# Performance work log

Measured on AMD Instinct MI355X. Metric: run time of the kernel, lower is better.

The kernel has to match this reference:

```python
import jax, jax.numpy as jnp
import numpy as np

B, N, C = 128, 36, 1024
K_NB = 16            # neighbors per node (top-k, includes loop)
KERNEL = 8           # number of Gaussian kernels
OUT = 1024           # out_dim; per-kernel out = OUT // KERNEL
PI = np.float32(np.pi)


def setup_inputs() -> dict:
    key = jax.random.key(0)
    ks = jax.random.split(key, 9)
    node_feats = jax.random.normal(ks[0], (B, N, C), dtype=jnp.float32)
    node_centre = jax.random.uniform(ks[1], (B, N, 2), dtype=jnp.float32)
    neighbor_idx = jax.random.randint(ks[2], (B * N, K_NB), 0, B * N, dtype=jnp.int32)
    graph_weights = jax.random.uniform(ks[3], (B * N * K_NB, 1), dtype=jnp.float32)
    # Gaussian kernel params (per reset_parameters)
    mean_rho = jax.random.uniform(ks[4], (1, KERNEL), dtype=jnp.float32)
    mean_theta = jax.random.uniform(ks[5], (1, KERNEL), minval=-PI, maxval=PI, dtype=jnp.float32)
    precision_rho = jax.random.uniform(ks[6], (1, KERNEL), minval=0.5, maxval=1.0, dtype=jnp.float32)
    precision_theta = jax.random.uniform(ks[7], (1, KERNEL), minval=0.5, maxval=1.0, dtype=jnp.float32)
    # per-kernel Linear(node_dim, out_dim//kernel, bias=False), stacked: [K, d_out_k, C]
    conv_w = jax.random.normal(ks[8], (KERNEL, OUT // KERNEL, C), dtype=jnp.float32) * (1.0 / np.sqrt(C))
    return {
        "node_feats": node_feats,
        "node_centre": node_centre,
        "neighbor_idx": neighbor_idx,
        "graph_weights": graph_weights,
        "mean_rho": mean_rho,
        "mean_theta": mean_theta,
        "precision_rho": precision_rho,
        "precision_theta": precision_theta,
        "conv_w": conv_w,
    }


def _forward(node_feats, node_centre, graph_weights,
             mean_rho, mean_theta, precision_rho, precision_theta,
             conv_w, neighbor_idx):
    b, n, c = node_feats.shape
    bn = b * n
    # pseudo polar coordinates per edge: centre_i - centre_j
    centre = node_centre.reshape(bn, 2)                       # [BN, 2]
    diff = centre[:, None, :] - centre[neighbor_idx]          # [BN, K_nb, 2]
    coord_x = diff[..., 0].reshape(-1)                        # [E]
    coord_y = diff[..., 1].reshape(-1)
    rho = jnp.sqrt(coord_x ** 2 + coord_y ** 2)
    theta = jnp.arctan2(coord_x, coord_y)
    # Gaussian mixture membership weights over KERNEL kernels
    w_rho = jnp.exp(-0.5 * (rho[:, None] - mean_rho) ** 2 / (1e-14 + precision_rho ** 2))
    first_angle = jnp.abs(theta[:, None] - mean_theta)
    second_angle = jnp.abs(2.0 * PI - first_angle)
    w_theta = jnp.exp(-0.5 * jnp.minimum(first_angle, second_angle) ** 2 / (1e-14 + precision_theta ** 2))
    weights = w_rho * w_theta                                  # [E, KERNEL]
    weights = jnp.where(jnp.isnan(weights), 0.0, weights)
    weights = weights / jnp.sum(weights, axis=1, keepdims=True)
    # combine with graph edge weights
    edge_w = graph_weights * weights                           # [E, KERNEL]
    edge_w = edge_w.reshape(bn, K_NB, KERNEL).transpose(0, 2, 1)  # [BN, K, K_nb]
    # gather neighbor features and weighted aggregate (bmm)
    nbr = node_feats.reshape(bn, c)[neighbor_idx]              # [BN, K_nb, C]
    agg = jnp.einsum('ekn,enc->ekc', edge_w, nbr)              # [BN, KERNEL, C]
    agg = agg.reshape(b, n, KERNEL, c)
    # per-kernel linear then concat over kernel dim
    out = jnp.einsum('bnkc,kdc->bnkd', agg, conv_w)            # [B, N, KERNEL, OUT//KERNEL]
    out = out.reshape(b, n, -1)                                # [B, N, OUT]
    return jax.nn.relu(out)


def reference(node_feats, node_centre, neighbor_idx, graph_weights,
              mean_rho, mean_theta, precision_rho, precision_theta, conv_w):
    return _forward(node_feats, node_centre, graph_weights,
                    mean_rho, mean_theta, precision_rho, precision_theta,
                    conv_w, neighbor_idx)
```

## Files before the change

kernel.cpp:

```cpp
#include <hip/hip_runtime.h>
#include <hip/hip_bf16.h>
#include <stdint.h>

#define B_DIM   128
#define N_DIM   36
#define C_DIM   1024
#define KNB     16
#define NKER    8
#define OUTD    1024
#define BN_NODES (B_DIM * N_DIM)
#define E_EDGES  (BN_NODES * KNB)
#define PI_F 3.14159265358979323846f

typedef __attribute__((ext_vector_type(8))) short bf16x8;
typedef __attribute__((ext_vector_type(4))) float floatx4;

struct alignas(8) U16x4 { unsigned short x, y, z, w; };

__device__ __forceinline__ unsigned short f2bf(float f) {
  union { float f; uint32_t u; } v; v.f = f;
  uint32_t u = v.u;
  return (unsigned short)((u + 0x7fffu + ((u >> 16) & 1u)) >> 16);
}
__device__ __forceinline__ float bf2f(unsigned short h) {
  union { uint32_t u; float f; } v; v.u = ((uint32_t)h) << 16;
  return v.f;
}

__device__ __forceinline__ void gload16(const void* g, void* l) {
  __builtin_amdgcn_global_load_lds((__attribute__((address_space(1))) void*)(g),
                                   (__attribute__((address_space(3))) void*)(l),
                                   16, 0, 0);
}

#define VMCNT(n) asm volatile("s_waitcnt vmcnt(" #n ")" ::: "memory")
#define LGKM0()  asm volatile("s_waitcnt lgkmcnt(0)" ::: "memory")

__global__ __launch_bounds__(256)
void cast_kernel(const float* __restrict__ feats,
                 const float* __restrict__ cw,
                 unsigned short* __restrict__ fb,
                 unsigned short* __restrict__ wb)
{
  const int NF4 = (BN_NODES * C_DIM) / 4;
  const int NW4 = (C_DIM * OUTD) / 4;
  int tid = blockIdx.x * 256 + threadIdx.x;
  if (tid < NF4) {
    float4 v = ((const float4*)feats)[tid];
    U16x4 o = { f2bf(v.x), f2bf(v.y), f2bf(v.z), f2bf(v.w) };
    ((U16x4*)fb)[tid] = o;
  } else {
    int t = tid - NF4;
    if (t < NW4) {
      float4 v = ((const float4*)cw)[t];
      U16x4 o = { f2bf(v.x), f2bf(v.y), f2bf(v.z), f2bf(v.w) };
      ((U16x4*)wb)[t] = o;
    }
  }
}

__global__ __launch_bounds__(256)
void gemm_bt(const unsigned short* __restrict__ A,
             const unsigned short* __restrict__ Bt,
             unsigned short* __restrict__ D)
{
  __shared__ unsigned short At [4][128 * 32];
  __shared__ unsigned short Bts[4][128 * 32];

  const int tid  = threadIdx.x;
  const int lane = tid & 63;
  const int wave = tid >> 6;
  const int wr   = wave >> 1;
  const int wc   = wave & 1;
  const int row0 = blockIdx.x * 128;
  const int col0 = blockIdx.y * 128;

  floatx4 acc[4][4] = {};

  const int r0 = tid >> 2, q = tid & 3;
  const int r1 = r0 + 64;

  const unsigned short* Ag0 = A  + (size_t)(row0 + r0) * C_DIM + q * 8;
  const unsigned short* Ag1 = A  + (size_t)(row0 + r1) * C_DIM + q * 8;
  const unsigned short* Bg0 = Bt + (size_t)(col0 + r0) * C_DIM + q * 8;
  const unsigned short* Bg1 = Bt + (size_t)(col0 + r1) * C_DIM + q * 8;

  const int qk = (lane >> 4) << 3;
  const int lr = lane & 15;

#define STAGE(s, k0) do {                              \
    gload16(Ag0 + (k0), &At [s][tid * 8]);             \
    gload16(Ag1 + (k0), &At [s][(tid + 256) * 8]);     \
    gload16(Bg0 + (k0), &Bts[s][tid * 8]);             \
    gload16(Bg1 + (k0), &Bts[s][(tid + 256) * 8]);     \
  } while (0)

#define FRAGS(s)                                                           \
    bf16x8 af[4], bfr[4];                                                  \
    _Pragma("unroll") for (int i = 0; i < 4; ++i) {                        \
      af[i]  = *(const bf16x8*)&At [s][(wr * 64 + i * 16 + lr) * 32 + qk]; \
      bfr[i] = *(const bf16x8*)&Bts[s][(wc * 64 + i * 16 + lr) * 32 + qk]; \
    }

#define MFMAS()                                                            \
    _Pragma("unroll") for (int i = 0; i < 4; ++i)                          \
    _Pragma("unroll") for (int j = 0; j < 4; ++j)                          \
      acc[i][j] = __builtin_amdgcn_mfma_f32_16x16x32_bf16(af[i], bfr[j], acc[i][j], 0, 0, 0);

  STAGE(0, 0); STAGE(1, 32); STAGE(2, 64); STAGE(3, 96);

#pragma unroll 4
  for (int it = 0; it < 28; ++it) {
    const int s = it & 3;
    VMCNT(12);
    __builtin_amdgcn_s_barrier();
    FRAGS(s);
    LGKM0();
    __builtin_amdgcn_s_barrier();
    STAGE(s, (it + 4) * 32);
    MFMAS();
  }
  { VMCNT(12); __builtin_amdgcn_s_barrier(); FRAGS(0); MFMAS(); }
  { VMCNT(8);  __builtin_amdgcn_s_barrier(); FRAGS(1); MFMAS(); }
  { VMCNT(4);  __builtin_amdgcn_s_barrier(); FRAGS(2); MFMAS(); }
  { VMCNT(0);  __builtin_amdgcn_s_barrier(); FRAGS(3); MFMAS(); }

  const int quad = lane >> 4;
#pragma unroll
  for (int i = 0; i < 4; ++i)
#pragma unroll
    for (int j = 0; j < 4; ++j)
#pragma unroll
      for (int r = 0; r < 4; ++r) {
        int row = row0 + wr * 64 + i * 16 + quad * 4 + r;
        int col = col0 + wc * 64 + j * 16 + lr;
        D[(size_t)row * OUTD + col] = f2bf(acc[i][j][r]);
      }
#undef STAGE
#undef FRAGS
#undef MFMAS
}

__global__ __launch_bounds__(256)
void agg_fused(const unsigned short* __restrict__ proj,
               const float* __restrict__ centre,
               const int*   __restrict__ nbr,
               const float* __restrict__ gw,
               const float* __restrict__ mrho,
               const float* __restrict__ mth,
               const float* __restrict__ prho,
               const float* __restrict__ pth,
               float* __restrict__ out)
{
  __shared__ int   idx[KNB];
  __shared__ float nx[KNB], ny[KNB];
  __shared__ float cc[2];
  __shared__ float wk[KNB][NKER];
  __shared__ float scl[KNB];
  __shared__ float ew[NKER][KNB];

  const int n = blockIdx.x;
  const int t = threadIdx.x;

  if (t < KNB) {
    int m = nbr[n * KNB + t];
    idx[t] = m;
    nx[t] = centre[2 * m];
    ny[t] = centre[2 * m + 1];
  } else if (t == KNB) {
    cc[0] = centre[2 * n];
    cc[1] = centre[2 * n + 1];
  }
  __syncthreads();

  if (t < 128) {
    int j = t >> 3, k = t & 7;
    float cx = cc[0] - nx[j];
    float cy = cc[1] - ny[j];
    float rho   = sqrtf(cx * cx + cy * cy);
    float theta = atan2f(cx, cy);
    float dr = rho - mrho[k];
    float pr = prho[k];
    float w_r = expf(-0.5f * dr * dr / (1e-14f + pr * pr));
    float fa = fabsf(theta - mth[k]);
    float sa = fabsf(2.0f * PI_F - fa);
    float mm = fminf(fa, sa);
    float pt = pth[k];
    float w_t = expf(-0.5f * mm * mm / (1e-14f + pt * pt));
    float ww = w_r * w_t;
    wk[j][k] = (ww != ww) ? 0.f : ww;
  }
  __syncthreads();

  if (t < KNB) {
    float s = 0.f;
#pragma unroll
    for (int k = 0; k < NKER; ++k) s += wk[t][k];
    scl[t] = gw[n * KNB + t] / s;
  }
  __syncthreads();

  if (t < 128) {
    int j = t >> 3, k = t & 7;
    ew[k][j] = wk[j][k] * scl[j];
  }
  __syncthreads();

  const int k = t >> 5;
  float a0 = 0.f, a1 = 0.f, a2 = 0.f, a3 = 0.f;
#pragma unroll
  for (int j = 0; j < KNB; ++j) {
    float wv = ew[k][j];
    U16x4 v = *(const U16x4*)&proj[(size_t)idx[j] * OUTD + t * 4];
    a0 += wv * bf2f(v.x);
    a1 += wv * bf2f(v.y);
    a2 += wv * bf2f(v.z);
    a3 += wv * bf2f(v.w);
  }
  float4 r;
  r.x = fmaxf(a0, 0.f); r.y = fmaxf(a1, 0.f);
  r.z = fmaxf(a2, 0.f); r.w = fmaxf(a3, 0.f);
  ((float4*)out)[(size_t)n * (OUTD / 4) + t] = r;
}

extern "C" void kernel_launch(void* const* d_in, const int* in_sizes, int n_in,
                              void* d_out, int out_size, void* d_ws, size_t ws_size,
                              hipStream_t stream)
{
  const float* feats  = (const float*)d_in[0];
  const float* centre = (const float*)d_in[1];
  const int*   nbr    = (const int*)  d_in[2];
  const float* gw     = (const float*)d_in[3];
  const float* mrho   = (const float*)d_in[4];
  const float* mth    = (const float*)d_in[5];
  const float* prho   = (const float*)d_in[6];
  const float* pth    = (const float*)d_in[7];
  const float* cw     = (const float*)d_in[8];
  float* out = (float*)d_out;

  char* ws = (char*)d_ws;
  unsigned short* fb   = (unsigned short*)(ws);
  unsigned short* wb   = (unsigned short*)(ws + 9437184);
  unsigned short* proj = (unsigned short*)(ws + 11534336);

  cast_kernel<<<dim3(((BN_NODES * C_DIM) / 4 + (C_DIM * OUTD) / 4) / 256),
                dim3(256), 0, stream>>>(feats, cw, fb, wb);
  gemm_bt<<<dim3(BN_NODES / 128, OUTD / 128), dim3(256), 0, stream>>>(fb, wb, proj);
  agg_fused<<<dim3(BN_NODES), dim3(256), 0, stream>>>(
      proj, centre, nbr, gw, mrho, mth, prho, pth, out);
}
```

Baseline: 128.0 us.

## Retile GEMM to 64x128 with register-staged double-buffered padded LDS

Replaces the 128x128 GEMM tile, which used a 4-stage direct global-to-LDS pipeline, with a 64x128 tile and BK=64. Global loads now go through registers into double-buffered LDS whose rows are padded to cut bank conflicts. The smaller tile doubles the grid (72x8 blocks) so more CUs are busy on this modest GEMM, and each block needs one fewer barrier per step. In exchange, per-block reuse drops, register pressure rises, and the explicit prefetch pipeline depth becomes shallower.

```diff
diff --git a/kernel.cpp b/kernel.cpp
--- a/kernel.cpp
+++ b/kernel.cpp
@@ -12,6 +12,12 @@
 #define E_EDGES  (BN_NODES * KNB)
 #define PI_F 3.14159265358979323846f
 
+#define TM  64
+#define TN  128
+#define BK  64
+#define LDP 72
+#define KITERS (C_DIM / BK)
+
 typedef __attribute__((ext_vector_type(8))) short bf16x8;
 typedef __attribute__((ext_vector_type(4))) float floatx4;
 
@@ -27,14 +33,9 @@
   return v.f;
 }
 
-__device__ __forceinline__ void gload16(const void* g, void* l) {
-  __builtin_amdgcn_global_load_lds((__attribute__((address_space(1))) void*)(g),
-                                   (__attribute__((address_space(3))) void*)(l),
-                                   16, 0, 0);
-}
-
-#define VMCNT(n) asm volatile("s_waitcnt vmcnt(" #n ")" ::: "memory")
-#define LGKM0()  asm volatile("s_waitcnt lgkmcnt(0)" ::: "memory")
+__device__ __forceinline__ void bar_sync() {
+  asm volatile("s_waitcnt lgkmcnt(0)\n\ts_barrier" ::: "memory");
+}
 
 __global__ __launch_bounds__(256)
 void cast_kernel(const float* __restrict__ feats,
@@ -64,81 +65,110 @@
              const unsigned short* __restrict__ Bt,
              unsigned short* __restrict__ D)
 {
-  __shared__ unsigned short At [4][128 * 32];
-  __shared__ unsigned short Bts[4][128 * 32];
+  __shared__ unsigned short Alds[2 * TM * LDP];
+  __shared__ unsigned short Blds[2 * TN * LDP];
 
   const int tid  = threadIdx.x;
   const int lane = tid & 63;
   const int wave = tid >> 6;
-  const int wr   = wave >> 1;
-  const int wc   = wave & 1;
-  const int row0 = blockIdx.x * 128;
-  const int col0 = blockIdx.y * 128;
-
-  floatx4 acc[4][4] = {};
-
-  const int r0 = tid >> 2, q = tid & 3;
-  const int r1 = r0 + 64;
-
-  const unsigned short* Ag0 = A  + (size_t)(row0 + r0) * C_DIM + q * 8;
-  const unsigned short* Ag1 = A  + (size_t)(row0 + r1) * C_DIM + q * 8;
-  const unsigned short* Bg0 = Bt + (size_t)(col0 + r0) * C_DIM + q * 8;
-  const unsigned short* Bg1 = Bt + (size_t)(col0 + r1) * C_DIM + q * 8;
+  const int wm   = wave >> 1;
+  const int wn   = wave & 1;
+  const int row0 = blockIdx.x * TM;
+  const int col0 = blockIdx.y * TN;
 
   const int qk = (lane >> 4) << 3;
   const int lr = lane & 15;
 
-#define STAGE(s, k0) do {                              \
-    gload16(Ag0 + (k0), &At [s][tid * 8]);             \
-    gload16(Ag1 + (k0), &At [s][(tid + 256) * 8]);     \
-    gload16(Bg0 + (k0), &Bts[s][tid * 8]);             \
-    gload16(Bg1 + (k0), &Bts[s][(tid + 256) * 8]);     \
+  floatx4 acc[2][4] = {};
+
+  const unsigned short* Ag = A  + (size_t)row0 * C_DIM;
+  const unsigned short* Bg = Bt + (size_t)col0 * C_DIM;
+
+  const int ac0 = tid, ac1 = tid + 256;
+  const size_t aG0 = (size_t)(ac0 >> 3) * C_DIM + (ac0 & 7) * 8;
+  const size_t aG1 = (size_t)(ac1 >> 3) * C_DIM + (ac1 & 7) * 8;
+  const int    aL0 = (ac0 >> 3) * LDP + (ac0 & 7) * 8;
+  const int    aL1 = (ac1 >> 3) * LDP + (ac1 & 7) * 8;
+
+  size_t bG[4]; int bL[4];
+#pragma unroll
+  for (int p = 0; p < 4; ++p) {
+    int c = tid + 256 * p;
+    bG[p] = (size_t)(c >> 3) * C_DIM + (c & 7) * 8;
+    bL[p] = (c >> 3) * LDP + (c & 7) * 8;
+  }
+
+  uint4 ra[2][2];
+  uint4 rb[2][4];
+
+#define LOADT(S, KT) do {                                         \
+    const unsigned short* ap = Ag + (size_t)(KT) * BK;            \
+    const unsigned short* bp = Bg + (size_t)(KT) * BK;            \
+    ra[S][0] = *(const uint4*)(ap + aG0);                         \
+    ra[S][1] = *(const uint4*)(ap + aG1);                         \
+    _Pragma("unroll") for (int p = 0; p < 4; ++p)                 \
+      rb[S][p] = *(const uint4*)(bp + bG[p]);                     \
   } while (0)
 
-#define FRAGS(s)                                                           \
-    bf16x8 af[4], bfr[4];                                                  \
-    _Pragma("unroll") for (int i = 0; i < 4; ++i) {                        \
-      af[i]  = *(const bf16x8*)&At [s][(wr * 64 + i * 16 + lr) * 32 + qk]; \
-      bfr[i] = *(const bf16x8*)&Bts[s][(wc * 64 + i * 16 + lr) * 32 + qk]; \
+#define STORET(S, BUF) do {                                       \
+    *(uint4*)&Alds[(BUF) * TM * LDP + aL0] = ra[S][0];            \
+    *(uint4*)&Alds[(BUF) * TM * LDP + aL1] = ra[S][1];            \
+    _Pragma("unroll") for (int p = 0; p < 4; ++p)                 \
+      *(uint4*)&Blds[(BUF) * TN * LDP + bL[p]] = rb[S][p];        \
+  } while (0)
+
+  LOADT(0, 0);
+  LOADT(1, 1);
+  STORET(0, 0);
+  bar_sync();
+
+  for (int it = 0; it < KITERS; it += 2) {
+#pragma unroll
+    for (int u = 0; u < 2; ++u) {
+      const int i2 = it + u;
+      const int P  = u;
+
+      bf16x8 af[2][2], bb[4][2];
+#pragma unroll
+      for (int i = 0; i < 2; ++i)
+#pragma unroll
+        for (int h = 0; h < 2; ++h)
+          af[i][h] = *(const bf16x8*)&Alds[P * TM * LDP +
+                       (wm * 32 + i * 16 + lr) * LDP + h * 32 + qk];
+#pragma unroll
+      for (int j = 0; j < 4; ++j)
+#pragma unroll
+        for (int h = 0; h < 2; ++h)
+          bb[j][h] = *(const bf16x8*)&Blds[P * TN * LDP +
+                       (wn * 64 + j * 16 + lr) * LDP + h * 32 + qk];
+
+      if (i2 + 2 < KITERS) LOADT(P, i2 + 2);
+      if (i2 + 1 < KITERS) { STORET(1 - P, 1 - P); bar_sync(); }
+
+#pragma unroll
+      for (int i = 0; i < 2; ++i)
+#pragma unroll
+        for (int j = 0; j < 4; ++j)
+#pragma unroll
+          for (int h = 0; h < 2; ++h)
+            acc[i][j] = __builtin_amdgcn_mfma_f32_16x16x32_bf16(
+                af[i][h], bb[j][h], acc[i][j], 0, 0, 0);
     }
-
-#define MFMAS()                                                            \
-    _Pragma("unroll") for (int i = 0; i < 4; ++i)                          \
-    _Pragma("unroll") for (int j = 0; j < 4; ++j)                          \
-      acc[i][j] = __builtin_amdgcn_mfma_f32_16x16x32_bf16(af[i], bfr[j], acc[i][j], 0, 0, 0);
-
-  STAGE(0, 0); STAGE(1, 32); STAGE(2, 64); STAGE(3, 96);
-
-#pragma unroll 4
-  for (int it = 0; it < 28; ++it) {
-    const int s = it & 3;
-    VMCNT(12);
-    __builtin_amdgcn_s_barrier();
-    FRAGS(s);
-    LGKM0();
-    __builtin_amdgcn_s_barrier();
-    STAGE(s, (it + 4) * 32);
-    MFMAS();
-  }
-  { VMCNT(12); __builtin_amdgcn_s_barrier(); FRAGS(0); MFMAS(); }
-  { VMCNT(8);  __builtin_amdgcn_s_barrier(); FRAGS(1); MFMAS(); }
-  { VMCNT(4);  __builtin_amdgcn_s_barrier(); FRAGS(2); MFMAS(); }
-  { VMCNT(0);  __builtin_amdgcn_s_barrier(); FRAGS(3); MFMAS(); }
+  }
+#undef LOADT
+#undef STORET
 
   const int quad = lane >> 4;
 #pragma unroll
-  for (int i = 0; i < 4; ++i)
+  for (int i = 0; i < 2; ++i)
 #pragma unroll
     for (int j = 0; j < 4; ++j)
 #pragma unroll
       for (int r = 0; r < 4; ++r) {
-        int row = row0 + wr * 64 + i * 16 + quad * 4 + r;
-        int col = col0 + wc * 64 + j * 16 + lr;
+        int row = row0 + wm * 32 + i * 16 + quad * 4 + r;
+        int col = col0 + wn * 64 + j * 16 + lr;
         D[(size_t)row * OUTD + col] = f2bf(acc[i][j][r]);
       }
-#undef STAGE
-#undef FRAGS
-#undef MFMAS
 }
 
 __global__ __launch_bounds__(256)
@@ -245,7 +275,7 @@
 
   cast_kernel<<<dim3(((BN_NODES * C_DIM) / 4 + (C_DIM * OUTD) / 4) / 256),
                 dim3(256), 0, stream>>>(feats, cw, fb, wb);
-  gemm_bt<<<dim3(BN_NODES / 128, OUTD / 128), dim3(256), 0, stream>>>(fb, wb, proj);
+  gemm_bt<<<dim3(BN_NODES / TM, OUTD / TN), dim3(256), 0, stream>>>(fb, wb, proj);
   agg_fused<<<dim3(BN_NODES), dim3(256), 0, stream>>>(
       proj, centre, nbr, gw, mrho, mth, prho, pth, out);
 }
```

Result: slower. 186.6 us (+45.8%).

## Rework GEMM to single-buffered BK=128 tiles with XOR swizzle and LDS-staged stores

Applied to the files above, without the earlier changes.

Replaces the 4-stage K=32 pipelined GEMM mainloop with a single-buffered loop that loads 128-wide K tiles into LDS using an XOR swizzle to avoid bank conflicts, then syncs and runs the MFMAs. The epilogue now stages the bf16 results through padded LDS and writes 16-byte coalesced rows instead of scattered 2-byte stores. This removes bank conflicts and uncoalesced stores but gives up the overlap between global loads and compute, since each tile is loaded and then waited on.

```diff
diff --git a/kernel.cpp b/kernel.cpp
--- a/kernel.cpp
+++ b/kernel.cpp
@@ -12,6 +12,11 @@
 #define E_EDGES  (BN_NODES * KNB)
 #define PI_F 3.14159265358979323846f
 
+#define TM 128
+#define TN 128
+#define BK 128
+#define CLP 136
+
 typedef __attribute__((ext_vector_type(8))) short bf16x8;
 typedef __attribute__((ext_vector_type(4))) float floatx4;
 
@@ -32,9 +37,6 @@
                                    (__attribute__((address_space(3))) void*)(l),
                                    16, 0, 0);
 }
-
-#define VMCNT(n) asm volatile("s_waitcnt vmcnt(" #n ")" ::: "memory")
-#define LGKM0()  asm volatile("s_waitcnt lgkmcnt(0)" ::: "memory")
 
 __global__ __launch_bounds__(256)
 void cast_kernel(const float* __restrict__ feats,
@@ -64,81 +66,77 @@
              const unsigned short* __restrict__ Bt,
              unsigned short* __restrict__ D)
 {
-  __shared__ unsigned short At [4][128 * 32];
-  __shared__ unsigned short Bts[4][128 * 32];
+  __shared__ unsigned short smem[TM * BK + TN * BK];
+  unsigned short* Al = smem;
+  unsigned short* Bl = smem + TM * BK;
 
   const int tid  = threadIdx.x;
   const int lane = tid & 63;
   const int wave = tid >> 6;
   const int wr   = wave >> 1;
   const int wc   = wave & 1;
-  const int row0 = blockIdx.x * 128;
-  const int col0 = blockIdx.y * 128;
+  const int row0 = blockIdx.x * TM;
+  const int col0 = blockIdx.y * TN;
+
+  const int q  = lane >> 4;
+  const int lr = lane & 15;
 
   floatx4 acc[4][4] = {};
 
-  const int r0 = tid >> 2, q = tid & 3;
-  const int r1 = r0 + 64;
-
-  const unsigned short* Ag0 = A  + (size_t)(row0 + r0) * C_DIM + q * 8;
-  const unsigned short* Ag1 = A  + (size_t)(row0 + r1) * C_DIM + q * 8;
-  const unsigned short* Bg0 = Bt + (size_t)(col0 + r0) * C_DIM + q * 8;
-  const unsigned short* Bg1 = Bt + (size_t)(col0 + r1) * C_DIM + q * 8;
-
-  const int qk = (lane >> 4) << 3;
-  const int lr = lane & 15;
-
-#define STAGE(s, k0) do {                              \
-    gload16(Ag0 + (k0), &At [s][tid * 8]);             \
-    gload16(Ag1 + (k0), &At [s][(tid + 256) * 8]);     \
-    gload16(Bg0 + (k0), &Bts[s][tid * 8]);             \
-    gload16(Bg1 + (k0), &Bts[s][(tid + 256) * 8]);     \
-  } while (0)
-
-#define FRAGS(s)                                                           \
-    bf16x8 af[4], bfr[4];                                                  \
-    _Pragma("unroll") for (int i = 0; i < 4; ++i) {                        \
-      af[i]  = *(const bf16x8*)&At [s][(wr * 64 + i * 16 + lr) * 32 + qk]; \
-      bfr[i] = *(const bf16x8*)&Bts[s][(wc * 64 + i * 16 + lr) * 32 + qk]; \
+  int offA[8], offB[8];
+#pragma unroll
+  for (int i = 0; i < 8; ++i) {
+    int c   = tid + 256 * i;
+    int row = c >> 4, qc = c & 15;
+    int sw  = qc ^ (row & 15);
+    offA[i] = (row0 + row) * C_DIM + sw * 8;
+    offB[i] = (col0 + row) * C_DIM + sw * 8;
+  }
+
+  for (int k0 = 0; k0 < C_DIM; k0 += BK) {
+#pragma unroll
+    for (int i = 0; i < 8; ++i) {
+      gload16(A  + offA[i] + k0, &Al[(tid + 256 * i) * 8]);
+      gload16(Bt + offB[i] + k0, &Bl[(tid + 256 * i) * 8]);
     }
-
-#define MFMAS()                                                            \
-    _Pragma("unroll") for (int i = 0; i < 4; ++i)                          \
-    _Pragma("unroll") for (int j = 0; j < 4; ++j)                          \
-      acc[i][j] = __builtin_amdgcn_mfma_f32_16x16x32_bf16(af[i], bfr[j], acc[i][j], 0, 0, 0);
-
-  STAGE(0, 0); STAGE(1, 32); STAGE(2, 64); STAGE(3, 96);
-
-#pragma unroll 4
-  for (int it = 0; it < 28; ++it) {
-    const int s = it & 3;
-    VMCNT(12);
-    __builtin_amdgcn_s_barrier();
-    FRAGS(s);
-    LGKM0();
-    __builtin_amdgcn_s_barrier();
-    STAGE(s, (it + 4) * 32);
-    MFMAS();
-  }
-  { VMCNT(12); __builtin_amdgcn_s_barrier(); FRAGS(0); MFMAS(); }
-  { VMCNT(8);  __builtin_amdgcn_s_barrier(); FRAGS(1); MFMAS(); }
-  { VMCNT(4);  __builtin_amdgcn_s_barrier(); FRAGS(2); MFMAS(); }
-  { VMCNT(0);  __builtin_amdgcn_s_barrier(); FRAGS(3); MFMAS(); }
-
-  const int quad = lane >> 4;
+    __syncthreads();
+
+#pragma unroll
+    for (int kc = 0; kc < 4; ++kc) {
+      const int sc = ((kc * 4 + q) ^ lr) * 8;
+      bf16x8 af[4], bfr[4];
+#pragma unroll
+      for (int i = 0; i < 4; ++i) {
+        af[i]  = *(const bf16x8*)&Al[(wr * 64 + i * 16 + lr) * BK + sc];
+        bfr[i] = *(const bf16x8*)&Bl[(wc * 64 + i * 16 + lr) * BK + sc];
+      }
+#pragma unroll
+      for (int i = 0; i < 4; ++i)
+#pragma unroll
+        for (int j = 0; j < 4; ++j)
+          acc[i][j] = __builtin_amdgcn_mfma_f32_16x16x32_bf16(
+              af[i], bfr[j], acc[i][j], 0, 0, 0);
+    }
+    __syncthreads();
+  }
+
+  unsigned short* Cl = smem;
 #pragma unroll
   for (int i = 0; i < 4; ++i)
 #pragma unroll
     for (int j = 0; j < 4; ++j)
 #pragma unroll
-      for (int r = 0; r < 4; ++r) {
-        int row = row0 + wr * 64 + i * 16 + quad * 4 + r;
-        int col = col0 + wc * 64 + j * 16 + lr;
-        D[(size_t)row * OUTD + col] = f2bf(acc[i][j][r]);
-      }
-#undef STAGE
-#undef FRAGS
-#undef MFMAS
+      for (int r = 0; r < 4; ++r)
+        Cl[(wr * 64 + i * 16 + q * 4 + r) * CLP + wc * 64 + j * 16 + lr] =
+            f2bf(acc[i][j][r]);
+  __syncthreads();
+#pragma unroll
+  for (int i = 0; i < 8; ++i) {
+    int c = tid + 256 * i;
+    int row = c >> 4, qc = c & 15;
+    *(uint4*)&D[(size_t)(row0 + row) * OUTD + col0 + qc * 8] =
+        *(const uint4*)&Cl[row * CLP + qc * 8];
+  }
 }
 
 __global__ __launch_bounds__(256)
@@ -245,7 +243,7 @@
 
   cast_kernel<<<dim3(((BN_NODES * C_DIM) / 4 + (C_DIM * OUTD) / 4) / 256),
                 dim3(256), 0, stream>>>(feats, cw, fb, wb);
-  gemm_bt<<<dim3(BN_NODES / 128, OUTD / 128), dim3(256), 0, stream>>>(fb, wb, proj);
+  gemm_bt<<<dim3(BN_NODES / TM, OUTD / TN), dim3(256), 0, stream>>>(fb, wb, proj);
   agg_fused<<<dim3(BN_NODES), dim3(256), 0, stream>>>(
       proj, centre, nbr, gw, mrho, mth, prho, pth, out);
 }
```

Result: no change. 126.9 us (-0.9%).
